# Kernel tuning notes

Hardware: AMD Instinct MI355X
Metric: run time of the kernel (lower is better)

Reference implementation:

```python
import jax, jax.numpy as jnp
import numpy as np

SCALE = 0.125          # feature stride 8
OUT = 7                # roi_align output size
SR = 2                 # sampling_ratio
BBW = (10.0, 10.0, 5.0, 5.0)   # torchvision BoxCoder weights
CLAMP = float(np.log(1000.0 / 16.0))
IMG_H, IMG_W = 800.0, 1088.0


def _bilinear(img, ys, xs):
    # img [C,H,W]; ys,xs [P] -> [C,P]
    C, H, W = img.shape
    y = jnp.clip(ys, 0.0, H - 1.0)
    x = jnp.clip(xs, 0.0, W - 1.0)
    y0 = jnp.floor(y); x0 = jnp.floor(x)
    y0i = y0.astype(jnp.int32); x0i = x0.astype(jnp.int32)
    y1i = jnp.minimum(y0i + 1, H - 1); x1i = jnp.minimum(x0i + 1, W - 1)
    ly = y - y0; lx = x - x0
    flat = img.reshape(C, H * W)
    g = lambda yi, xi: flat[:, yi * W + xi]
    return (g(y0i, x0i) * (1 - ly) * (1 - lx) + g(y0i, x1i) * (1 - ly) * lx
            + g(y1i, x0i) * ly * (1 - lx) + g(y1i, x1i) * ly * lx)


def _roi_align(features, boxes, roi_batch):
    # features [B,C,H,W], boxes [N,4] (image coords), roi_batch [N] -> [N,C,7,7]
    B, C, H, W = features.shape
    P = OUT * SR

    def one(b, box):
        x1, y1, x2, y2 = box[0] * SCALE, box[1] * SCALE, box[2] * SCALE, box[3] * SCALE
        rw = jnp.maximum(x2 - x1, 1.0)
        rh = jnp.maximum(y2 - y1, 1.0)
        bw = rw / OUT; bh = rh / OUT
        off = (jnp.arange(OUT)[:, None] + (jnp.arange(SR)[None, :] + 0.5) / SR).reshape(-1)  # [P]
        ys = y1 + off * bh
        xs = x1 + off * bw
        yy = jnp.repeat(ys, P)   # [P*P], y-major
        xx = jnp.tile(xs, P)
        v = _bilinear(features[b], yy, xx)                   # [C, P*P]
        return v.reshape(C, OUT, SR, OUT, SR).mean(axis=(2, 4))  # avg over samples

    return jax.vmap(one)(roi_batch, boxes)


def _decode(deltas, boxes):
    # deltas [N,K,4], boxes [N,4] -> [N,K,4]
    pw = boxes[:, 2] - boxes[:, 0]
    ph = boxes[:, 3] - boxes[:, 1]
    cx = boxes[:, 0] + 0.5 * pw
    cy = boxes[:, 1] + 0.5 * ph
    dx = deltas[..., 0] / BBW[0]; dy = deltas[..., 1] / BBW[1]
    dw = jnp.minimum(deltas[..., 2] / BBW[2], CLAMP)
    dh = jnp.minimum(deltas[..., 3] / BBW[3], CLAMP)
    pcx = dx * pw[:, None] + cx[:, None]
    pcy = dy * ph[:, None] + cy[:, None]
    pww = jnp.exp(dw) * pw[:, None]
    phh = jnp.exp(dh) * ph[:, None]
    out = jnp.stack([
        jnp.clip(pcx - 0.5 * pww, 0.0, IMG_W),
        jnp.clip(pcy - 0.5 * phh, 0.0, IMG_H),
        jnp.clip(pcx + 0.5 * pww, 0.0, IMG_W),
        jnp.clip(pcy + 0.5 * phh, 0.0, IMG_H),
    ], axis=-1)
    return out


def setup_inputs() -> dict:
    key = jax.random.key(0)
    ks = jax.random.split(key, 12)
    B, C, H, W, N, NC = 2, 256, 100, 136, 1000, 2
    features = jax.random.normal(ks[0], (B, C, H, W), jnp.float32)
    # valid proposal boxes in image coords
    cx = jax.random.uniform(ks[1], (N,)) * IMG_W
    cy = jax.random.uniform(ks[2], (N,)) * IMG_H
    bw = jax.random.uniform(ks[3], (N,)) * 240.0 + 16.0
    bh = jax.random.uniform(ks[4], (N,)) * 240.0 + 16.0
    x1 = jnp.clip(cx - 0.5 * bw, 0.0, IMG_W - 2.0)
    y1 = jnp.clip(cy - 0.5 * bh, 0.0, IMG_H - 2.0)
    x2 = jnp.clip(x1 + bw, x1 + 1.0, IMG_W - 1.0)
    y2 = jnp.clip(y1 + bh, y1 + 1.0, IMG_H - 1.0)
    boxes = jnp.stack([x1, y1, x2, y2], axis=-1).astype(jnp.float32)
    roi_batch = jax.random.randint(ks[5], (N,), 0, B, dtype=jnp.int32)
    D = C * OUT * OUT  # 12544
    HID = 1024
    s = 0.02
    fc1_w = jax.random.normal(ks[6], (D, HID), jnp.float32) * s
    fc1_b = jnp.zeros((HID,), jnp.float32)
    fc2_w = jax.random.normal(ks[7], (HID, HID), jnp.float32) * s
    fc2_b = jnp.zeros((HID,), jnp.float32)
    cls_w = jax.random.normal(ks[8], (HID, NC), jnp.float32) * s
    cls_b = jnp.zeros((NC,), jnp.float32)
    bbox_w = jax.random.normal(ks[9], (HID, NC * 4), jnp.float32) * s
    bbox_b = jnp.zeros((NC * 4,), jnp.float32)
    return {"features": features, "boxes": boxes, "roi_batch": roi_batch,
            "fc1_w": fc1_w, "fc1_b": fc1_b, "fc2_w": fc2_w, "fc2_b": fc2_b,
            "cls_w": cls_w, "cls_b": cls_b, "bbox_w": bbox_w, "bbox_b": bbox_b}


def reference(features, boxes, roi_batch, fc1_w, fc1_b, fc2_w, fc2_b, cls_w, cls_b, bbox_w, bbox_b):
    N = boxes.shape[0]
    feats = _roi_align(features, boxes, roi_batch).reshape(N, -1)  # [N, 12544]
    h = jax.nn.relu(feats @ fc1_w + fc1_b)                         # TwoMLPHead fc6
    h = jax.nn.relu(h @ fc2_w + fc2_b)                             # TwoMLPHead fc7
    scores = jax.nn.softmax(h @ cls_w + cls_b, axis=-1)            # [N, 2]
    deltas = (h @ bbox_w + bbox_b).reshape(N, -1, 4)               # [N, 2, 4]
    dec = _decode(deltas, boxes).reshape(N, -1)                    # [N, 8]
    return jnp.concatenate([dec, scores], axis=-1)                 # [N, 10]
```

## Files before the change

kernel.cpp:

```cpp
#include <hip/hip_runtime.h>
#include <hip/hip_bf16.h>

#define BF16 __hip_bfloat16

typedef __bf16 bf16x8 __attribute__((ext_vector_type(8)));
typedef float floatx4 __attribute__((ext_vector_type(4)));

struct __align__(8) bf4 { BF16 a, b, c, d; };

__device__ __forceinline__ void glds16(const void* g, void* l) {
    __builtin_amdgcn_global_load_lds(
        (const __attribute__((address_space(1))) void*)g,
        (__attribute__((address_space(3))) void*)l, 16, 0, 0);
}

__global__ __launch_bounds__(256) void transpose_cvt(const float* __restrict__ in,
                                                     BF16* __restrict__ out,
                                                     int R, int C) {
    __shared__ float tile[32][33];
    size_t boff = (size_t)blockIdx.z * R * C;
    const float* ip = in + boff;
    BF16* op = out + boff;
    int tx = threadIdx.x & 31, ty = threadIdx.x >> 5;
    int r0 = blockIdx.y << 5, c0 = blockIdx.x << 5;
#pragma unroll
    for (int i = 0; i < 4; ++i)
        tile[ty + i * 8][tx] = ip[(size_t)(r0 + ty + i * 8) * C + c0 + tx];
    __syncthreads();
#pragma unroll
    for (int i = 0; i < 4; ++i)
        op[(size_t)(c0 + ty + i * 8) * R + r0 + tx] = __float2bfloat16(tile[tx][ty + i * 8]);
}

__global__ __launch_bounds__(256) void roi_align_k(const BF16* __restrict__ featT,
                                                   const float* __restrict__ boxes,
                                                   const int* __restrict__ roi_batch,
                                                   BF16* __restrict__ feats) {
    __shared__ __align__(16) int   s_off[196][4];
    __shared__ __align__(16) float s_w[196][4];
    __shared__ BF16 lbuf[12544];
    int roi = blockIdx.x;
    int t = threadIdx.x;
    BF16* orow = feats + (size_t)roi * 12544;
    if (roi >= 1000) {
        uint* o4 = (uint*)orow;
        for (int i = t; i < 6272; i += 256) o4[i] = 0u;
        return;
    }
    int b = roi_batch[roi];

    if (t < 196) {
        float x1 = boxes[roi * 4 + 0] * 0.125f;
        float y1 = boxes[roi * 4 + 1] * 0.125f;
        float x2 = boxes[roi * 4 + 2] * 0.125f;
        float y2 = boxes[roi * 4 + 3] * 0.125f;
        float bw = fmaxf(x2 - x1, 1.0f) * (1.0f / 7.0f);
        float bh = fmaxf(y2 - y1, 1.0f) * (1.0f / 7.0f);
        int cell = t >> 2, s = t & 3;
        int oy = cell / 7, ox = cell - oy * 7;
        int sy = s >> 1, sx = s & 1;
        float yc = y1 + ((float)oy + ((float)sy + 0.5f) * 0.5f) * bh;
        float xc = x1 + ((float)ox + ((float)sx + 0.5f) * 0.5f) * bw;
        yc = fminf(fmaxf(yc, 0.0f), 99.0f);
        xc = fminf(fmaxf(xc, 0.0f), 135.0f);
        float y0f = floorf(yc), x0f = floorf(xc);
        int y0 = (int)y0f, x0 = (int)x0f;
        int y1i = min(y0 + 1, 99), x1i = min(x0 + 1, 135);
        float ly = yc - y0f, lx = xc - x0f;
        s_w[t][0] = (1.0f - ly) * (1.0f - lx) * 0.25f;
        s_w[t][1] = (1.0f - ly) * lx * 0.25f;
        s_w[t][2] = ly * (1.0f - lx) * 0.25f;
        s_w[t][3] = ly * lx * 0.25f;
        s_off[t][0] = (y0 * 136 + x0) * 256;
        s_off[t][1] = (y0 * 136 + x1i) * 256;
        s_off[t][2] = (y1i * 136 + x0) * 256;
        s_off[t][3] = (y1i * 136 + x1i) * 256;
    }
    __syncthreads();

    int lane = t & 63, cg = t >> 6;
    const BF16* fb = featT + (size_t)b * (100 * 136 * 256) + lane * 4;
    int cbase = lane * 4;
    for (int cell = cg; cell < 49; cell += 4) {
        float a0 = 0.f, a1 = 0.f, a2 = 0.f, a3 = 0.f;
#pragma unroll
        for (int s = 0; s < 4; ++s) {
            int p = cell * 4 + s;
#pragma unroll
            for (int tap = 0; tap < 4; ++tap) {
                float w = s_w[p][tap];
                bf4 v = *(const bf4*)(fb + s_off[p][tap]);
                a0 += w * __bfloat162float(v.a);
                a1 += w * __bfloat162float(v.b);
                a2 += w * __bfloat162float(v.c);
                a3 += w * __bfloat162float(v.d);
            }
        }
        lbuf[(cbase + 0) * 49 + cell] = __float2bfloat16(a0);
        lbuf[(cbase + 1) * 49 + cell] = __float2bfloat16(a1);
        lbuf[(cbase + 2) * 49 + cell] = __float2bfloat16(a2);
        lbuf[(cbase + 3) * 49 + cell] = __float2bfloat16(a3);
    }
    __syncthreads();
    uint* o4 = (uint*)orow;
    const uint* l4 = (const uint*)lbuf;
    for (int i = t; i < 6272; i += 256) o4[i] = l4[i];
}

__global__ __launch_bounds__(256) void gemm_splitk(const BF16* __restrict__ A,
                                                   const BF16* __restrict__ Bt,
                                                   float* __restrict__ P,
                                                   int K, int chunk) {
    __shared__ char lds[2][2][8192];
    int w = threadIdx.x >> 6, l = threadIdx.x & 63;
    int wm = w & 1, wn = w >> 1;
    int tm = blockIdx.y, tn = blockIdx.x, s = blockIdx.z;
    int k0 = s * chunk;

    floatx4 acc[4][4];
#pragma unroll
    for (int i = 0; i < 4; ++i)
#pragma unroll
        for (int j = 0; j < 4; ++j) acc[i][j] = (floatx4){0.f, 0.f, 0.f, 0.f};

    const size_t strideA = (size_t)K * 2;
    const char* gA = (const char*)A + (size_t)(tm * 128 + w * 16 + (l >> 2)) * strideA
                     + (size_t)k0 * 2 + (size_t)(l & 3) * 16;
    const char* gB = (const char*)Bt + (size_t)(tn * 128 + w * 16 + (l >> 2)) * strideA
                     + (size_t)k0 * 2 + (size_t)(l & 3) * 16;
    size_t rowJump = 64 * strideA;

    int aoff = (wm * 64 + (l & 15)) * 64 + (l >> 4) * 16;
    int boff = (wn * 64 + (l & 15)) * 64 + (l >> 4) * 16;

    int nIter = chunk >> 5;

    glds16(gA, &lds[0][0][w * 1024]);
    glds16(gA + rowJump, &lds[0][0][w * 1024 + 4096]);
    glds16(gB, &lds[0][1][w * 1024]);
    glds16(gB + rowJump, &lds[0][1][w * 1024 + 4096]);
    __syncthreads();

    for (int kb = 0; kb < nIter; ++kb) {
        int cur = kb & 1;
        if (kb + 1 < nIter) {
            const char* pa = gA + (size_t)(kb + 1) * 64;
            const char* pb = gB + (size_t)(kb + 1) * 64;
            char* la = &lds[cur ^ 1][0][w * 1024];
            char* lb = &lds[cur ^ 1][1][w * 1024];
            glds16(pa, la);
            glds16(pa + rowJump, la + 4096);
            glds16(pb, lb);
            glds16(pb + rowJump, lb + 4096);
        }
        const char* bufA = lds[cur][0];
        const char* bufB = lds[cur][1];
        bf16x8 af[4], bf[4];
#pragma unroll
        for (int mi = 0; mi < 4; ++mi) af[mi] = *(const bf16x8*)(bufA + aoff + mi * 1024);
#pragma unroll
        for (int ni = 0; ni < 4; ++ni) bf[ni] = *(const bf16x8*)(bufB + boff + ni * 1024);
#pragma unroll
        for (int mi = 0; mi < 4; ++mi)
#pragma unroll
            for (int ni = 0; ni < 4; ++ni)
                acc[mi][ni] = __builtin_amdgcn_mfma_f32_16x16x32_bf16(af[mi], bf[ni], acc[mi][ni], 0, 0, 0);
        __syncthreads();
    }

    int q = l >> 4, c = l & 15;
    size_t base = (size_t)s << 20;
#pragma unroll
    for (int mi = 0; mi < 4; ++mi) {
        int rowG = tm * 128 + wm * 64 + mi * 16 + q * 4;
#pragma unroll
        for (int ni = 0; ni < 4; ++ni) {
            int colG = tn * 128 + wn * 64 + ni * 16 + c;
#pragma unroll
            for (int r = 0; r < 4; ++r)
                P[base + (size_t)(rowG + r) * 1024 + colG] = acc[mi][ni][r];
        }
    }
}

__global__ __launch_bounds__(256) void reduce_k(const float* __restrict__ P,
                                                const float* __restrict__ bias,
                                                BF16* __restrict__ out,
                                                int S, int relu) {
    int i = blockIdx.x * 256 + threadIdx.x;
    float a = bias[i & 1023];
    for (int s = 0; s < S; ++s) a += P[((size_t)s << 20) + i];
    if (relu) a = fmaxf(a, 0.0f);
    out[i] = __float2bfloat16(a);
}

__global__ __launch_bounds__(256) void head_k(const BF16* __restrict__ h2,
                                              const float* __restrict__ cls_w,
                                              const float* __restrict__ cls_b,
                                              const float* __restrict__ bbox_w,
                                              const float* __restrict__ bbox_b,
                                              const float* __restrict__ boxes,
                                              float* __restrict__ out) {
    int w = threadIdx.x >> 6, l = threadIdx.x & 63;
    int roi = blockIdx.x * 4 + w;
    if (roi >= 1000) return;
    float acc[10];
#pragma unroll
    for (int j = 0; j < 10; ++j) acc[j] = 0.0f;
    const BF16* hr = h2 + (size_t)roi * 1024;
    for (int k = l; k < 1024; k += 64) {
        float h = __bfloat162float(hr[k]);
        acc[0] += h * cls_w[k * 2 + 0];
        acc[1] += h * cls_w[k * 2 + 1];
#pragma unroll
        for (int j = 0; j < 8; ++j) acc[2 + j] += h * bbox_w[k * 8 + j];
    }
#pragma unroll
    for (int j = 0; j < 10; ++j) {
#pragma unroll
        for (int off = 32; off > 0; off >>= 1) acc[j] += __shfl_down(acc[j], off);
    }
    if (l == 0) {
        float s0 = acc[0] + cls_b[0], s1 = acc[1] + cls_b[1];
        float m = fmaxf(s0, s1);
        float e0 = expf(s0 - m), e1 = expf(s1 - m);
        float inv = 1.0f / (e0 + e1);

        float bx1 = boxes[roi * 4 + 0], by1 = boxes[roi * 4 + 1];
        float bx2 = boxes[roi * 4 + 2], by2 = boxes[roi * 4 + 3];
        float pw = bx2 - bx1, ph = by2 - by1;
        float cx = bx1 + 0.5f * pw, cy = by1 + 0.5f * ph;
        const float CLAMPV = 4.135166556742356f;
        float* orow = out + roi * 10;
#pragma unroll
        for (int cl = 0; cl < 2; ++cl) {
            float dx = (acc[2 + cl * 4 + 0] + bbox_b[cl * 4 + 0]) * 0.1f;
            float dy = (acc[2 + cl * 4 + 1] + bbox_b[cl * 4 + 1]) * 0.1f;
            float dw = fminf((acc[2 + cl * 4 + 2] + bbox_b[cl * 4 + 2]) * 0.2f, CLAMPV);
            float dh = fminf((acc[2 + cl * 4 + 3] + bbox_b[cl * 4 + 3]) * 0.2f, CLAMPV);
            float pcx = dx * pw + cx, pcy = dy * ph + cy;
            float pww = expf(dw) * pw, phh = expf(dh) * ph;
            orow[cl * 4 + 0] = fminf(fmaxf(pcx - 0.5f * pww, 0.0f), 1088.0f);
            orow[cl * 4 + 1] = fminf(fmaxf(pcy - 0.5f * phh, 0.0f), 800.0f);
            orow[cl * 4 + 2] = fminf(fmaxf(pcx + 0.5f * pww, 0.0f), 1088.0f);
            orow[cl * 4 + 3] = fminf(fmaxf(pcy + 0.5f * phh, 0.0f), 800.0f);
        }
        orow[8] = e0 * inv;
        orow[9] = e1 * inv;
    }
}

extern "C" void kernel_launch(void* const* d_in, const int* in_sizes, int n_in,
                              void* d_out, int out_size, void* d_ws, size_t ws_size,
                              hipStream_t stream) {
    const float* features = (const float*)d_in[0];
    const float* boxes    = (const float*)d_in[1];
    const int*   roi_b    = (const int*)d_in[2];
    const float* fc1_w    = (const float*)d_in[3];
    const float* fc1_b    = (const float*)d_in[4];
    const float* fc2_w    = (const float*)d_in[5];
    const float* fc2_b    = (const float*)d_in[6];
    const float* cls_w    = (const float*)d_in[7];
    const float* cls_b    = (const float*)d_in[8];
    const float* bbox_w   = (const float*)d_in[9];
    const float* bbox_b   = (const float*)d_in[10];
    float* out = (float*)d_out;

    char* ws = (char*)d_ws;
    BF16* featT = (BF16*)(ws + 0);
    BF16* w1t   = (BF16*)(ws + 13926400);
    BF16* w2t   = (BF16*)(ws + 39616512);
    BF16* feats = (BF16*)(ws + 41713664);
    BF16* h1    = (BF16*)(ws + 67403776);
    BF16* h2    = (BF16*)(ws + 69500928);
    float* P    = (float*)(ws + 71598080);

    size_t avail = (ws_size > 71598080) ? ws_size - 71598080 : 0;
    int S = 8;
    if (avail < (size_t)8 * 4194304) S = 4;
    if (avail < (size_t)4 * 4194304) S = 2;

    transpose_cvt<<<dim3(425, 8, 2), 256, 0, stream>>>(features, featT, 256, 13600);
    transpose_cvt<<<dim3(32, 392, 1), 256, 0, stream>>>(fc1_w, w1t, 12544, 1024);
    transpose_cvt<<<dim3(32, 32, 1), 256, 0, stream>>>(fc2_w, w2t, 1024, 1024);

    roi_align_k<<<1024, 256, 0, stream>>>(featT, boxes, roi_b, feats);

    gemm_splitk<<<dim3(8, 8, S), 256, 0, stream>>>(feats, w1t, P, 12544, 12544 / S);
    reduce_k<<<4096, 256, 0, stream>>>(P, fc1_b, h1, S, 1);

    gemm_splitk<<<dim3(8, 8, S), 256, 0, stream>>>(h1, w2t, P, 1024, 1024 / S);
    reduce_k<<<4096, 256, 0, stream>>>(P, fc2_b, h2, S, 1);

    head_k<<<250, 256, 0, stream>>>(h2, cls_w, cls_b, bbox_w, bbox_b, boxes, out);
}
```

Baseline: 244.2 us.

## Merge transposes, store bf16 split-K partials, fuse fc2 reduce into head

Combines the three transpose/convert launches into one kernel that selects its source from the block index. Split-K partials are now stored as bf16 instead of fp32, and fc1 split-K rises to 14. The fc2 partial reduction, bias and ReLU are folded into the head kernel, which removes a launch and an intermediate buffer. In exchange, the bf16 partial sums lose accuracy, and the fc2 partial buffer reuses workspace that held the transposed features.

```diff
diff --git a/kernel.cpp b/kernel.cpp
--- a/kernel.cpp
+++ b/kernel.cpp
@@ -14,15 +14,36 @@
         (__attribute__((address_space(3))) void*)l, 16, 0, 0);
 }
 
-__global__ __launch_bounds__(256) void transpose_cvt(const float* __restrict__ in,
-                                                     BF16* __restrict__ out,
-                                                     int R, int C) {
+__global__ __launch_bounds__(256) void transpose_all(const float* __restrict__ features,
+                                                     const float* __restrict__ fc1_w,
+                                                     const float* __restrict__ fc2_w,
+                                                     BF16* __restrict__ featT,
+                                                     BF16* __restrict__ w1t,
+                                                     BF16* __restrict__ w2t) {
     __shared__ float tile[32][33];
-    size_t boff = (size_t)blockIdx.z * R * C;
-    const float* ip = in + boff;
-    BF16* op = out + boff;
+    int bid = blockIdx.x;
+    const float* ip;
+    BF16* op;
+    int R, C, cx, cy;
+    if (bid < 6800) {
+        int z = bid / 3400, r = bid - z * 3400;
+        cx = r % 425; cy = r / 425;
+        R = 256; C = 13600;
+        ip = features + (size_t)z * 256 * 13600;
+        op = featT + (size_t)z * 256 * 13600;
+    } else if (bid < 19344) {
+        int r = bid - 6800;
+        cx = r & 31; cy = r >> 5;
+        R = 12544; C = 1024;
+        ip = fc1_w; op = w1t;
+    } else {
+        int r = bid - 19344;
+        cx = r & 31; cy = r >> 5;
+        R = 1024; C = 1024;
+        ip = fc2_w; op = w2t;
+    }
     int tx = threadIdx.x & 31, ty = threadIdx.x >> 5;
-    int r0 = blockIdx.y << 5, c0 = blockIdx.x << 5;
+    int r0 = cy << 5, c0 = cx << 5;
 #pragma unroll
     for (int i = 0; i < 4; ++i)
         tile[ty + i * 8][tx] = ip[(size_t)(r0 + ty + i * 8) * C + c0 + tx];
@@ -109,7 +130,7 @@
 
 __global__ __launch_bounds__(256) void gemm_splitk(const BF16* __restrict__ A,
                                                    const BF16* __restrict__ Bt,
-                                                   float* __restrict__ P,
+                                                   BF16* __restrict__ P,
                                                    int K, int chunk) {
     __shared__ char lds[2][2][8192];
     int w = threadIdx.x >> 6, l = threadIdx.x & 63;
@@ -178,38 +199,41 @@
             int colG = tn * 128 + wn * 64 + ni * 16 + c;
 #pragma unroll
             for (int r = 0; r < 4; ++r)
-                P[base + (size_t)(rowG + r) * 1024 + colG] = acc[mi][ni][r];
+                P[base + (size_t)(rowG + r) * 1024 + colG] = __float2bfloat16(acc[mi][ni][r]);
         }
     }
 }
 
-__global__ __launch_bounds__(256) void reduce_k(const float* __restrict__ P,
+__global__ __launch_bounds__(256) void reduce_k(const BF16* __restrict__ P,
                                                 const float* __restrict__ bias,
                                                 BF16* __restrict__ out,
-                                                int S, int relu) {
+                                                int S) {
     int i = blockIdx.x * 256 + threadIdx.x;
     float a = bias[i & 1023];
-    for (int s = 0; s < S; ++s) a += P[((size_t)s << 20) + i];
-    if (relu) a = fmaxf(a, 0.0f);
+    for (int s = 0; s < S; ++s) a += __bfloat162float(P[((size_t)s << 20) + i]);
+    a = fmaxf(a, 0.0f);
     out[i] = __float2bfloat16(a);
 }
 
-__global__ __launch_bounds__(256) void head_k(const BF16* __restrict__ h2,
+__global__ __launch_bounds__(256) void head_k(const BF16* __restrict__ P2,
+                                              const float* __restrict__ fc2_b,
                                               const float* __restrict__ cls_w,
                                               const float* __restrict__ cls_b,
                                               const float* __restrict__ bbox_w,
                                               const float* __restrict__ bbox_b,
                                               const float* __restrict__ boxes,
-                                              float* __restrict__ out) {
+                                              float* __restrict__ out, int S2) {
     int w = threadIdx.x >> 6, l = threadIdx.x & 63;
     int roi = blockIdx.x * 4 + w;
     if (roi >= 1000) return;
     float acc[10];
 #pragma unroll
     for (int j = 0; j < 10; ++j) acc[j] = 0.0f;
-    const BF16* hr = h2 + (size_t)roi * 1024;
+    const BF16* pr = P2 + (size_t)roi * 1024;
     for (int k = l; k < 1024; k += 64) {
-        float h = __bfloat162float(hr[k]);
+        float h = fc2_b[k];
+        for (int s = 0; s < S2; ++s) h += __bfloat162float(pr[((size_t)s << 20) + k]);
+        h = fmaxf(h, 0.0f);
         acc[0] += h * cls_w[k * 2 + 0];
         acc[1] += h * cls_w[k * 2 + 1];
 #pragma unroll
@@ -272,25 +296,20 @@
     BF16* w2t   = (BF16*)(ws + 39616512);
     BF16* feats = (BF16*)(ws + 41713664);
     BF16* h1    = (BF16*)(ws + 67403776);
-    BF16* h2    = (BF16*)(ws + 69500928);
-    float* P    = (float*)(ws + 71598080);
-
-    size_t avail = (ws_size > 71598080) ? ws_size - 71598080 : 0;
-    int S = 8;
-    if (avail < (size_t)8 * 4194304) S = 4;
-    if (avail < (size_t)4 * 4194304) S = 2;
-
-    transpose_cvt<<<dim3(425, 8, 2), 256, 0, stream>>>(features, featT, 256, 13600);
-    transpose_cvt<<<dim3(32, 392, 1), 256, 0, stream>>>(fc1_w, w1t, 12544, 1024);
-    transpose_cvt<<<dim3(32, 32, 1), 256, 0, stream>>>(fc2_w, w2t, 1024, 1024);
+    BF16* P1    = (BF16*)(ws + 69500928);
+    BF16* P2    = (BF16*)(ws + 0);
+
+    int S1 = (ws_size >= (size_t)69500928 + (size_t)14 * 2097152) ? 14 : 8;
+    int S2 = 8;
+
+    transpose_all<<<20368, 256, 0, stream>>>(features, fc1_w, fc2_w, featT, w1t, w2t);
 
     roi_align_k<<<1024, 256, 0, stream>>>(featT, boxes, roi_b, feats);
 
-    gemm_splitk<<<dim3(8, 8, S), 256, 0, stream>>>(feats, w1t, P, 12544, 12544 / S);
-    reduce_k<<<4096, 256, 0, stream>>>(P, fc1_b, h1, S, 1);
-
-    gemm_splitk<<<dim3(8, 8, S), 256, 0, stream>>>(h1, w2t, P, 1024, 1024 / S);
-    reduce_k<<<4096, 256, 0, stream>>>(P, fc2_b, h2, S, 1);
-
-    head_k<<<250, 256, 0, stream>>>(h2, cls_w, cls_b, bbox_w, bbox_b, boxes, out);
-}
+    gemm_splitk<<<dim3(8, 8, S1), 256, 0, stream>>>(feats, w1t, P1, 12544, 12544 / S1);
+    reduce_k<<<4096, 256, 0, stream>>>(P1, fc1_b, h1, S1);
+
+    gemm_splitk<<<dim3(8, 8, S2), 256, 0, stream>>>(h1, w2t, P2, 1024, 1024 / S2);
+
+    head_k<<<250, 256, 0, stream>>>(P2, fc2_b, cls_w, cls_b, bbox_w, bbox_b, boxes, out, S2);
+}
```

After: 261.8 us. +7.2%, slower.
